# Optimization experiments

Measured on AMD Instinct MI355X. Metric: run time of the kernel, lower is better.

Reference implementation:

```python
import jax, jax.numpy as jnp
import numpy as np

K = 5  # filter_size
EPS = 1e-5

def conv1x1(x, w):
    # x: [B,Ci,H,W], w: [Co,Ci]
    return jnp.einsum('bihw,oi->bohw', x, w)

def layernorm_c(x, g, b):
    # LayerNorm over channel dim of NCHW (torch permutes to NHWC, norms last dim)
    m = x.mean(axis=1, keepdims=True)
    v = x.var(axis=1, keepdims=True)
    xn = (x - m) / jnp.sqrt(v + EPS)
    return xn * g[None, :, None, None] + b[None, :, None, None]

def conv3x3(x, w):
    return jax.lax.conv_general_dilated(x, w, (1, 1), [(1, 1), (1, 1)],
                                        dimension_numbers=('NCHW', 'OIHW', 'NCHW'))

def apply_dyn_filter(feat, filt):
    # feat: [B,C,H,W]; filt: [B,C*K*K,H,W] ordered as C x (K*K row-major), matching
    # torch .view(B,C,K*K,H,W) and F.unfold channel layout.
    B, C, H, W = feat.shape
    f = filt.reshape(B, C, K * K, H, W)
    p = K // 2
    fp = jnp.pad(feat, ((0, 0), (0, 0), (p, p), (p, p)))  # zero pad, same as F.unfold
    out = jnp.zeros_like(feat)
    for ki in range(K):
        for kj in range(K):
            out = out + fp[:, :, ki:ki + H, kj:kj + W] * f[:, :, ki * K + kj]
    return out


def setup_inputs() -> dict:
    key = jax.random.key(0)
    ks = jax.random.split(key, 9)
    B, Cin, H, W = 1, 64, 128, 128
    Ch = 128
    s = lambda fan: 1.0 / np.sqrt(fan)
    inp = {
        'rgb_high': jax.random.normal(ks[0], (B, Cin, H, W), jnp.float32),
        'event':    jax.random.normal(ks[1], (B, Cin, H, W), jnp.float32),
        'conv_w':   jax.random.normal(ks[2], (Ch, Cin), jnp.float32) * s(Cin),
        'ln_g':     jnp.ones((Ch,), jnp.float32),
        'ln_b':     jnp.zeros((Ch,), jnp.float32),
        'df1_w':    jax.random.normal(ks[3], (Ch, Ch, 3, 3), jnp.float32) * s(Ch * 9),
        'df2_w':    jax.random.normal(ks[4], (Ch * K * K, Ch), jnp.float32) * s(Ch),
        'sp_w':     jax.random.normal(ks[5], (Ch, Ch), jnp.float32) * s(Ch),
        'out_w':    jax.random.normal(ks[6], (Cin, Ch), jnp.float32) * s(Ch),
    }
    return inp


def reference(rgb_high, event, conv_w, ln_g, ln_b, df1_w, df2_w, sp_w, out_w):
    rgb_feat = layernorm_c(conv1x1(rgb_high, conv_w), ln_g, ln_b)
    ev_feat = layernorm_c(conv1x1(event, conv_w), ln_g, ln_b)
    # dynamic filter generator: conv3x3 -> ReLU -> conv1x1 (shared weights)
    rgb_filter = conv1x1(jax.nn.relu(conv3x3(rgb_feat, df1_w)), df2_w)
    ev_filter = conv1x1(jax.nn.relu(conv3x3(ev_feat, df1_w)), df2_w)
    rgb_en = apply_dyn_filter(rgb_feat, rgb_filter)
    ev_en = apply_dyn_filter(ev_feat, ev_filter)
    rgb_filtered = rgb_en * jax.nn.sigmoid(conv1x1(ev_en, sp_w))
    rgb_fused = rgb_en + rgb_filtered + rgb_feat
    rgb_norm = layernorm_c(rgb_fused, ln_g, ln_b)
    return conv1x1(rgb_norm, out_w)
```

## Files before the change

kernel.cpp:

```cpp
#include <hip/hip_runtime.h>
#include <math.h>

#define HW 16384
#define WD 128
#define HD 128
#define CIN 64
#define CH 128
#define EPSV 1e-5f

typedef __attribute__((ext_vector_type(8))) short short8;
typedef __attribute__((ext_vector_type(4))) short short4v;
typedef __attribute__((ext_vector_type(4))) float f32x4;

__device__ __forceinline__ short f2bf(float x) {
  unsigned u = __float_as_uint(x);
  u += 0x7FFFu + ((u >> 16) & 1u);
  return (short)(u >> 16);
}
__device__ __forceinline__ float bf2f(short x) {
  return __uint_as_float(((unsigned)(unsigned short)x) << 16);
}

__global__ __launch_bounds__(256) void k_prep_all(
    const float* __restrict__ cw, const float* __restrict__ w3,
    const float* __restrict__ spw, const float* __restrict__ outw,
    const float* __restrict__ rgb, const float* __restrict__ ev,
    const float* __restrict__ df2,
    short* __restrict__ cwp, short* __restrict__ w3p,
    short* __restrict__ spwp, short* __restrict__ outwp,
    short* __restrict__ xT_rgb, short* __restrict__ xT_ev,
    short* __restrict__ df2p) {
  int idx = blockIdx.x * 256 + threadIdx.x;
  if (idx < 8192) {
    int j = idx & 7, grp = (idx >> 3) & 3, m = (idx >> 5) & 127, q = idx >> 12;
    cwp[idx] = f2bf(cw[m * CIN + q * 32 + grp * 8 + j]);
  } else if (idx < 155648) {
    int i = idx - 8192;
    int j = i & 7, grp = (i >> 3) & 3, m = (i >> 5) & 127, ks = i >> 12;
    int tap = ks >> 2, q = ks & 3;
    int c = q * 32 + grp * 8 + j;
    w3p[i] = f2bf(w3[(m * CH + c) * 9 + tap]);
  } else if (idx < 172032) {
    int i = idx - 155648;
    int j = i & 7, grp = (i >> 3) & 3, m = (i >> 5) & 127, q = i >> 12;
    spwp[i] = f2bf(spw[m * CH + q * 32 + grp * 8 + j]);
  } else if (idx < 180224) {
    int i = idx - 172032;
    int j = i & 7, grp = (i >> 3) & 3, m = (i >> 5) & 63, q = i >> 11;
    outwp[i] = f2bf(outw[m * CH + q * 32 + grp * 8 + j]);
  } else if (idx < 212992) {
    int i = idx - 180224;
    int img = i >> 14, p = i & 16383;
    const float* x = img ? ev : rgb;
    short* xT = img ? xT_ev : xT_rgb;
#pragma unroll
    for (int cb = 0; cb < 8; ++cb) {
      short8 v;
#pragma unroll
      for (int j = 0; j < 8; ++j) v[j] = f2bf(x[(cb * 8 + j) * HW + p]);
      *(short8*)(xT + p * CIN + cb * 8) = v;
    }
  } else {
    int i = idx - 212992;
    int j = i & 7;
    int slotp = (i >> 3) & 511;
    int c = i >> 12;
    int t = slotp >> 4, k8l = slotp & 15;
    int k8 = k8l ^ (t & 7);
    float v = (t < 25) ? df2[(c * 25 + t) * CH + k8 * 8 + j] : 0.f;
    df2p[i] = f2bf(v);
  }
}

__global__ __launch_bounds__(256) void k_feat_mfma(
    const short* __restrict__ xT_rgb, const short* __restrict__ xT_ev,
    const short* __restrict__ cwp, const float* __restrict__ g,
    const float* __restrict__ b,
    short* __restrict__ featT_rgb, short* __restrict__ featT_ev) {
  __shared__ float sg[CH], sb[CH];
  int tid = threadIdx.x;
  if (tid < CH) { sg[tid] = g[tid]; sb[tid] = b[tid]; }
  __syncthreads();
  const short* xT = blockIdx.z ? xT_ev : xT_rgb;
  short* featT = blockIdx.z ? featT_ev : featT_rgb;
  int wave = tid >> 6, lane = tid & 63, col = lane & 15, grp = lane >> 4;
  int p = blockIdx.x * 64 + wave * 16 + col;

  const short8* bp = (const short8*)(xT + p * CIN);
  short8 bq0 = bp[grp], bq1 = bp[4 + grp];
  const short8* ap = (const short8*)cwp;

  f32x4 acc[8];
#pragma unroll
  for (int mt = 0; mt < 8; ++mt) {
    acc[mt] = (f32x4){0.f, 0.f, 0.f, 0.f};
    short8 a0 = ap[(0 * 128 + mt * 16 + col) * 4 + grp];
    short8 a1 = ap[(1 * 128 + mt * 16 + col) * 4 + grp];
    acc[mt] = __builtin_amdgcn_mfma_f32_16x16x32_bf16(a0, bq0, acc[mt], 0, 0, 0);
    acc[mt] = __builtin_amdgcn_mfma_f32_16x16x32_bf16(a1, bq1, acc[mt], 0, 0, 0);
  }
  float s = 0.f, s2 = 0.f;
#pragma unroll
  for (int mt = 0; mt < 8; ++mt)
#pragma unroll
    for (int r = 0; r < 4; ++r) { float v = acc[mt][r]; s += v; s2 += v * v; }
  s += __shfl_xor(s, 16);  s += __shfl_xor(s, 32);
  s2 += __shfl_xor(s2, 16); s2 += __shfl_xor(s2, 32);
  float mean = s * (1.f / CH);
  float var = s2 * (1.f / CH) - mean * mean;
  float rinv = rsqrtf(var + EPSV);
#pragma unroll
  for (int mt = 0; mt < 8; ++mt) {
    short4v fv;
#pragma unroll
    for (int r = 0; r < 4; ++r) {
      int m = mt * 16 + grp * 4 + r;
      fv[r] = f2bf((acc[mt][r] - mean) * rinv * sg[m] + sb[m]);
    }
    *(short4v*)(featT + p * CH + mt * 16 + grp * 4) = fv;
  }
}

__global__ __launch_bounds__(256) void k_conv3_v3(
    const short* __restrict__ featT_rgb, const short* __restrict__ featT_ev,
    const short* __restrict__ w3p,
    short* __restrict__ rT_rgb, short* __restrict__ rT_ev) {
  const short* featT = blockIdx.z ? featT_ev : featT_rgb;
  short* rT = blockIdx.z ? rT_ev : rT_rgb;
  int tid = threadIdx.x, wave = tid >> 6, lane = tid & 63;
  int col = lane & 15, grp = lane >> 4;
  int mh = wave & 1;
  int ty = (blockIdx.x >> 3) * 4 + (wave >> 1) * 2;
  int tx = (blockIdx.x & 7) * 16;
  int x = tx + col;

  f32x4 acc[2][4];
#pragma unroll
  for (int s = 0; s < 2; ++s)
#pragma unroll
    for (int mt = 0; mt < 4; ++mt) acc[s][mt] = (f32x4){0.f, 0.f, 0.f, 0.f};

  const short8* ap = (const short8*)w3p;
#pragma unroll
  for (int ks = 0; ks < 36; ++ks) {
    const int tap = ks >> 2, q = ks & 3;
    const int dy = tap / 3 - 1, dx = tap % 3 - 1;
    int xs = x + dx;
    bool xok = (unsigned)xs < (unsigned)WD;
    int y0 = ty + dy, y1 = ty + 1 + dy;
    short8 b0 = {0, 0, 0, 0, 0, 0, 0, 0}, b1 = {0, 0, 0, 0, 0, 0, 0, 0};
    if (xok && (unsigned)y0 < (unsigned)HD)
      b0 = *(const short8*)(featT + (y0 * WD + xs) * CH + q * 32 + grp * 8);
    if (xok && (unsigned)y1 < (unsigned)HD)
      b1 = *(const short8*)(featT + (y1 * WD + xs) * CH + q * 32 + grp * 8);
#pragma unroll
    for (int mt = 0; mt < 4; ++mt) {
      short8 a = ap[(ks * 128 + (mh * 4 + mt) * 16 + col) * 4 + grp];
      acc[0][mt] = __builtin_amdgcn_mfma_f32_16x16x32_bf16(a, b0, acc[0][mt], 0, 0, 0);
      acc[1][mt] = __builtin_amdgcn_mfma_f32_16x16x32_bf16(a, b1, acc[1][mt], 0, 0, 0);
    }
  }
#pragma unroll
  for (int s = 0; s < 2; ++s) {
    int p = (ty + s) * WD + x;
#pragma unroll
    for (int mt = 0; mt < 4; ++mt) {
      short4v v;
#pragma unroll
      for (int r = 0; r < 4; ++r) v[r] = f2bf(fmaxf(acc[s][mt][r], 0.f));
      *(short4v*)(rT + p * CH + (mh * 4 + mt) * 16 + grp * 4) = v;
    }
  }
}

__global__ __launch_bounds__(256, 3) void k_filt_v6(
    const short* __restrict__ featT_rgb, const short* __restrict__ featT_ev,
    const short* __restrict__ rT_rgb, const short* __restrict__ rT_ev,
    const short* __restrict__ df2p,
    short* __restrict__ enT_rgb, short* __restrict__ enT_ev) {
  __shared__ short lsA[4 * 512 * 8];
  __shared__ float fwv[4 * 400 + 64];
  const short* featT = blockIdx.z ? featT_ev : featT_rgb;
  const short* rT = blockIdx.z ? rT_ev : rT_rgb;
  short* enT = blockIdx.z ? enT_ev : enT_rgb;
  int tid = threadIdx.x;
  int wave = tid >> 6, lane = tid & 63;
  int col = lane & 15, grp = lane >> 4;
  int ty0 = (blockIdx.x >> 3) * 16, tx0 = (blockIdx.x & 7) * 16;
  int c0 = blockIdx.y * 4;
  int py0 = ty0 + wave * 4;
  int pxx = tx0 + col;

  {
    const short8* gsrc = (const short8*)(df2p + (size_t)c0 * 4096);
    short8* lA = (short8*)lsA;
    for (int i = tid; i < 2048; i += 256) lA[i] = gsrc[i];
  }
  for (int px = tid; px < 400; px += 256) {
    int wr = px / 20, wc = px % 20;
    int y = ty0 + wr - 2, x = tx0 + wc - 2;
    short4v v = {0, 0, 0, 0};
    if ((unsigned)y < (unsigned)HD && (unsigned)x < (unsigned)WD)
      v = *(const short4v*)(featT + (y * WD + x) * CH + c0);
#pragma unroll
    for (int ci = 0; ci < 4; ++ci) fwv[ci * 400 + px] = bf2f(v[ci]);
  }
  if (tid < 64) fwv[4 * 400 + tid] = 0.f;

  short8 rv[4][4];
#pragma unroll
  for (int s = 0; s < 4; ++s) {
    const short8* bp = (const short8*)(rT + ((py0 + s) * WD + pxx) * CH);
#pragma unroll
    for (int q = 0; q < 4; ++q) rv[s][q] = bp[q * 4 + grp];
  }
#pragma unroll
  for (int s = 0; s < 4; ++s)
#pragma unroll
    for (int q = 0; q < 4; ++q) asm volatile("" :: "v"(rv[s][q]));

  int idx0[4], idx1[4];
#pragma unroll
  for (int r = 0; r < 4; ++r) {
    int tap0 = grp * 4 + r;
    int tap1 = 16 + grp * 4 + r;
    idx0[r] = (wave * 4 + tap0 / 5) * 20 + col + tap0 % 5;
    idx1[r] = (wave * 4 + tap1 / 5) * 20 + col + tap1 % 5;
  }
  __syncthreads();

  const short8* lA8 = (const short8*)lsA;
  short* stp = enT + ((py0 + grp) * WD + pxx) * CH + c0;
  short4v sv;

#pragma unroll
  for (int c = 0; c < 4; ++c) {
    int base0 = c * 512 + col * 16;
    int base1 = base0 + 256;
    short8 a[4];
    f32x4 acc0[4], acc1[4];
#pragma unroll
    for (int q = 0; q < 4; ++q) a[q] = lA8[base0 + (((q << 2) | grp) ^ (col & 7))];
#pragma unroll
    for (int s = 0; s < 4; ++s) {
      acc0[s] = (f32x4){0.f, 0.f, 0.f, 0.f};
#pragma unroll
      for (int q = 0; q < 4; ++q)
        acc0[s] = __builtin_amdgcn_mfma_f32_16x16x32_bf16(a[q], rv[s][q], acc0[s], 0, 0, 0);
    }
#pragma unroll
    for (int q = 0; q < 4; ++q) a[q] = lA8[base1 + (((q << 2) | grp) ^ (col & 7))];
#pragma unroll
    for (int s = 0; s < 4; ++s) {
      acc1[s] = (f32x4){0.f, 0.f, 0.f, 0.f};
#pragma unroll
      for (int q = 0; q < 4; ++q)
        acc1[s] = __builtin_amdgcn_mfma_f32_16x16x32_bf16(a[q], rv[s][q], acc1[s], 0, 0, 0);
    }
    const float* fwc = fwv + c * 400;
    float part[4];
#pragma unroll
    for (int s = 0; s < 4; ++s) {
      float p = 0.f;
#pragma unroll
      for (int r = 0; r < 4; ++r) {
        p += fwc[idx0[r] + s * 20] * acc0[s][r];
        p += fwc[idx1[r] + s * 20] * acc1[s][r];
      }
      part[s] = p;
    }
#pragma unroll
    for (int s = 0; s < 4; ++s) part[s] += __shfl_xor(part[s], 16);
#pragma unroll
    for (int s = 0; s < 4; ++s) part[s] += __shfl_xor(part[s], 32);
    float val = (grp == 0) ? part[0] : (grp == 1) ? part[1]
              : (grp == 2) ? part[2] : part[3];
    sv[c] = f2bf(val);
  }
  *(short4v*)stp = sv;
}

__global__ __launch_bounds__(256) void k_post(
    const short* __restrict__ enT_rgb, const short* __restrict__ enT_ev,
    const short* __restrict__ featT_rgb,
    const short* __restrict__ spwp, const short* __restrict__ outwp,
    const float* __restrict__ g, const float* __restrict__ b,
    float* __restrict__ out) {
  __shared__ short nlds[4][16 * 136];
  __shared__ float sg[CH], sb[CH];
  int tid = threadIdx.x;
  if (tid < CH) { sg[tid] = g[tid]; sb[tid] = b[tid]; }
  __syncthreads();
  int wave = tid >> 6, lane = tid & 63, col = lane & 15, grp = lane >> 4;
  int p = blockIdx.x * 64 + wave * 16 + col;

  const short8* bp = (const short8*)(enT_ev + p * CH);
  short8 bq[4];
#pragma unroll
  for (int q = 0; q < 4; ++q) bq[q] = bp[q * 4 + grp];
  const short8* ap = (const short8*)spwp;
  f32x4 z[8];
#pragma unroll
  for (int mt = 0; mt < 8; ++mt) {
    z[mt] = (f32x4){0.f, 0.f, 0.f, 0.f};
#pragma unroll
    for (int q = 0; q < 4; ++q)
      z[mt] = __builtin_amdgcn_mfma_f32_16x16x32_bf16(
          ap[(q * 128 + mt * 16 + col) * 4 + grp], bq[q], z[mt], 0, 0, 0);
  }

  const short4v* er = (const short4v*)(enT_rgb + p * CH);
  const short4v* fr = (const short4v*)(featT_rgb + p * CH);
  float fused[8][4];
  float s = 0.f, s2 = 0.f;
#pragma unroll
  for (int mt = 0; mt < 8; ++mt) {
    short4v e4 = er[mt * 4 + grp];
    short4v f4 = fr[mt * 4 + grp];
#pragma unroll
    for (int r = 0; r < 4; ++r) {
      float sig = 1.f / (1.f + __expf(-z[mt][r]));
      float f = bf2f(e4[r]) * (1.f + sig) + bf2f(f4[r]);
      fused[mt][r] = f; s += f; s2 += f * f;
    }
  }
  s += __shfl_xor(s, 16);  s += __shfl_xor(s, 32);
  s2 += __shfl_xor(s2, 16); s2 += __shfl_xor(s2, 32);
  float mean = s * (1.f / CH);
  float var = s2 * (1.f / CH) - mean * mean;
  float rinv = rsqrtf(var + EPSV);

  short* nl = &nlds[wave][0];
#pragma unroll
  for (int mt = 0; mt < 8; ++mt) {
    short4v nv;
#pragma unroll
    for (int r = 0; r < 4; ++r) {
      int o = mt * 16 + grp * 4 + r;
      nv[r] = f2bf((fused[mt][r] - mean) * rinv * sg[o] + sb[o]);
    }
    *(short4v*)(nl + col * 136 + mt * 16 + grp * 4) = nv;
  }

  short8 nb[4];
#pragma unroll
  for (int q = 0; q < 4; ++q)
    nb[q] = *(const short8*)(nl + col * 136 + q * 32 + grp * 8);
  const short8* op = (const short8*)outwp;
#pragma unroll
  for (int mt = 0; mt < 4; ++mt) {
    f32x4 oacc = {0.f, 0.f, 0.f, 0.f};
#pragma unroll
    for (int q = 0; q < 4; ++q)
      oacc = __builtin_amdgcn_mfma_f32_16x16x32_bf16(
          op[(q * 64 + mt * 16 + col) * 4 + grp], nb[q], oacc, 0, 0, 0);
#pragma unroll
    for (int r = 0; r < 4; ++r)
      out[(mt * 16 + grp * 4 + r) * HW + p] = oacc[r];
  }
}

extern "C" void kernel_launch(void* const* d_in, const int* in_sizes, int n_in,
                              void* d_out, int out_size, void* d_ws, size_t ws_size,
                              hipStream_t stream) {
  const float* rgb  = (const float*)d_in[0];
  const float* ev   = (const float*)d_in[1];
  const float* cw   = (const float*)d_in[2];
  const float* g    = (const float*)d_in[3];
  const float* b    = (const float*)d_in[4];
  const float* w3   = (const float*)d_in[5];
  const float* df2  = (const float*)d_in[6];
  const float* spw  = (const float*)d_in[7];
  const float* outw = (const float*)d_in[8];
  float* out = (float*)d_out;
  char* wsb = (char*)d_ws;

  const size_t MB = 1u << 20;
  short* featT_rgb = (short*)(wsb);
  short* featT_ev  = (short*)(wsb + 4 * MB);
  short* rT_rgb    = (short*)(wsb + 8 * MB);
  short* rT_ev     = (short*)(wsb + 12 * MB);
  short* enT_rgb   = (short*)(wsb + 16 * MB);
  short* enT_ev    = (short*)(wsb + 20 * MB);
  short* xT_rgb    = (short*)(wsb + 24 * MB);
  short* xT_ev     = (short*)(wsb + 26 * MB);
  short* df2p      = (short*)(wsb + 28 * MB);
  short* w3p       = (short*)(wsb + 29 * MB);
  short* cwp       = (short*)(wsb + 30 * MB);
  short* spwp      = (short*)(wsb + 31 * MB);
  short* outwp     = (short*)(wsb + 32 * MB);

  hipLaunchKernelGGL(k_prep_all, dim3(2880), dim3(256), 0, stream,
                     cw, w3, spw, outw, rgb, ev, df2,
                     cwp, w3p, spwp, outwp, xT_rgb, xT_ev, df2p);
  hipLaunchKernelGGL(k_feat_mfma, dim3(256, 1, 2), dim3(256), 0, stream,
                     xT_rgb, xT_ev, cwp, g, b, featT_rgb, featT_ev);
  hipLaunchKernelGGL(k_conv3_v3, dim3(256, 1, 2), dim3(256), 0, stream,
                     featT_rgb, featT_ev, w3p, rT_rgb, rT_ev);
  hipLaunchKernelGGL(k_filt_v6, dim3(64, 32, 2), dim3(256), 0, stream,
                     featT_rgb, featT_ev, rT_rgb, rT_ev, df2p, enT_rgb, enT_ev);
  hipLaunchKernelGGL(k_post, dim3(256), dim3(256), 0, stream,
                     enT_rgb, enT_ev, featT_rgb, spwp, outwp, g, b, out);
}
```

Before: 113.4 us.

## Switch dynamic-filter kernel to 32x32x16 MFMA with repacked tap layout

Rewrites the filter-generation-and-apply kernel to use 32x32x16 bf16 MFMA instead of 16x16x32. The 25 filter taps are repacked into 32 rows in a new order chosen to match the 32x32 output layout, and the B-operand loads cover two pixel rows per tile. The per-lane tap-weighted reduction now needs only one cross-lane shuffle instead of two, with fewer accumulator registers per output. The intent is higher MFMA throughput and less reduction and shuffle overhead. In exchange the tap indexing becomes harder to follow and more register tiles live at once.

```diff
diff --git a/kernel.cpp b/kernel.cpp
--- a/kernel.cpp
+++ b/kernel.cpp
@@ -11,6 +11,7 @@
 typedef __attribute__((ext_vector_type(8))) short short8;
 typedef __attribute__((ext_vector_type(4))) short short4v;
 typedef __attribute__((ext_vector_type(4))) float f32x4;
+typedef __attribute__((ext_vector_type(16))) float f32x16;
 
 __device__ __forceinline__ short f2bf(float x) {
   unsigned u = __float_as_uint(x);
@@ -65,9 +66,15 @@
     int j = i & 7;
     int slotp = (i >> 3) & 511;
     int c = i >> 12;
-    int t = slotp >> 4, k8l = slotp & 15;
-    int k8 = k8l ^ (t & 7);
-    float v = (t < 25) ? df2[(c * 25 + t) * CH + k8 * 8 + j] : 0.f;
+    int m = slotp >> 4, k8s = slotp & 15;
+    int k8 = k8s ^ (m & 7);
+    int k = k8 * 8 + j;
+    int t;
+    if (m < 20) t = (m >> 2) * 5 + (m & 3);
+    else if (m == 24) t = 24;
+    else if (m >= 28) t = (m - 28) * 5 + 4;
+    else t = -1;
+    float v = (t >= 0) ? df2[(c * 25 + t) * CH + k] : 0.f;
     df2p[i] = f2bf(v);
   }
 }
@@ -173,23 +180,25 @@
   }
 }
 
-__global__ __launch_bounds__(256, 3) void k_filt_v6(
+__global__ __launch_bounds__(256, 3) void k_filt_v11(
     const short* __restrict__ featT_rgb, const short* __restrict__ featT_ev,
     const short* __restrict__ rT_rgb, const short* __restrict__ rT_ev,
     const short* __restrict__ df2p,
     short* __restrict__ enT_rgb, short* __restrict__ enT_ev) {
   __shared__ short lsA[4 * 512 * 8];
-  __shared__ float fwv[4 * 400 + 64];
+  __shared__ float fwv[4 * 400];
   const short* featT = blockIdx.z ? featT_ev : featT_rgb;
   const short* rT = blockIdx.z ? rT_ev : rT_rgb;
   short* enT = blockIdx.z ? enT_ev : enT_rgb;
   int tid = threadIdx.x;
   int wave = tid >> 6, lane = tid & 63;
-  int col = lane & 15, grp = lane >> 4;
+  int hi = lane >> 5;
+  int n = lane & 31;
+  int rbit = (n >> 4) & 1;
+  int cc = n & 15;
   int ty0 = (blockIdx.x >> 3) * 16, tx0 = (blockIdx.x & 7) * 16;
   int c0 = blockIdx.y * 4;
   int py0 = ty0 + wave * 4;
-  int pxx = tx0 + col;
 
   {
     const short8* gsrc = (const short8*)(df2p + (size_t)c0 * 4096);
@@ -205,77 +214,62 @@
 #pragma unroll
     for (int ci = 0; ci < 4; ++ci) fwv[ci * 400 + px] = bf2f(v[ci]);
   }
-  if (tid < 64) fwv[4 * 400 + tid] = 0.f;
-
-  short8 rv[4][4];
-#pragma unroll
-  for (int s = 0; s < 4; ++s) {
-    const short8* bp = (const short8*)(rT + ((py0 + s) * WD + pxx) * CH);
-#pragma unroll
-    for (int q = 0; q < 4; ++q) rv[s][q] = bp[q * 4 + grp];
-  }
-#pragma unroll
-  for (int s = 0; s < 4; ++s)
-#pragma unroll
-    for (int q = 0; q < 4; ++q) asm volatile("" :: "v"(rv[s][q]));
-
-  int idx0[4], idx1[4];
-#pragma unroll
-  for (int r = 0; r < 4; ++r) {
-    int tap0 = grp * 4 + r;
-    int tap1 = 16 + grp * 4 + r;
-    idx0[r] = (wave * 4 + tap0 / 5) * 20 + col + tap0 % 5;
-    idx1[r] = (wave * 4 + tap1 / 5) * 20 + col + tap1 % 5;
-  }
+
+  short8 rv[2][8];
+#pragma unroll
+  for (int P = 0; P < 2; ++P) {
+    const short* bsrc = rT + ((py0 + 2 * P + rbit) * WD + tx0 + cc) * CH + hi * 8;
+#pragma unroll
+    for (int ks = 0; ks < 8; ++ks)
+      rv[P][ks] = *(const short8*)(bsrc + ks * 16);
+  }
+#pragma unroll
+  for (int P = 0; P < 2; ++P)
+#pragma unroll
+    for (int ks = 0; ks < 8; ++ks) asm volatile("" :: "v"(rv[P][ks]));
+
+  int fwb0 = (wave * 4 + rbit) * 20 + cc;
+  int q0o = 20 * hi;
+  int q1o = 40 + 20 * hi;
+  int q2o = hi ? 0 : 80;
+  int s0o = hi ? 4 : 84;
+  int s1o = hi ? 24 : 84;
+  int s2o = hi ? 44 : 84;
+  int s3o = hi ? 64 : 84;
   __syncthreads();
 
   const short8* lA8 = (const short8*)lsA;
-  short* stp = enT + ((py0 + grp) * WD + pxx) * CH + c0;
+  int sw = n & 7;
+  short* stp = enT + ((py0 + 2 * hi + rbit) * WD + tx0 + cc) * CH + c0;
   short4v sv;
 
 #pragma unroll
   for (int c = 0; c < 4; ++c) {
-    int base0 = c * 512 + col * 16;
-    int base1 = base0 + 256;
-    short8 a[4];
-    f32x4 acc0[4], acc1[4];
-#pragma unroll
-    for (int q = 0; q < 4; ++q) a[q] = lA8[base0 + (((q << 2) | grp) ^ (col & 7))];
-#pragma unroll
-    for (int s = 0; s < 4; ++s) {
-      acc0[s] = (f32x4){0.f, 0.f, 0.f, 0.f};
-#pragma unroll
-      for (int q = 0; q < 4; ++q)
-        acc0[s] = __builtin_amdgcn_mfma_f32_16x16x32_bf16(a[q], rv[s][q], acc0[s], 0, 0, 0);
-    }
-#pragma unroll
-    for (int q = 0; q < 4; ++q) a[q] = lA8[base1 + (((q << 2) | grp) ^ (col & 7))];
-#pragma unroll
-    for (int s = 0; s < 4; ++s) {
-      acc1[s] = (f32x4){0.f, 0.f, 0.f, 0.f};
-#pragma unroll
-      for (int q = 0; q < 4; ++q)
-        acc1[s] = __builtin_amdgcn_mfma_f32_16x16x32_bf16(a[q], rv[s][q], acc1[s], 0, 0, 0);
-    }
-    const float* fwc = fwv + c * 400;
-    float part[4];
-#pragma unroll
-    for (int s = 0; s < 4; ++s) {
-      float p = 0.f;
-#pragma unroll
-      for (int r = 0; r < 4; ++r) {
-        p += fwc[idx0[r] + s * 20] * acc0[s][r];
-        p += fwc[idx1[r] + s * 20] * acc1[s][r];
-      }
-      part[s] = p;
-    }
-#pragma unroll
-    for (int s = 0; s < 4; ++s) part[s] += __shfl_xor(part[s], 16);
-#pragma unroll
-    for (int s = 0; s < 4; ++s) part[s] += __shfl_xor(part[s], 32);
-    float val = (grp == 0) ? part[0] : (grp == 1) ? part[1]
-              : (grp == 2) ? part[2] : part[3];
-    sv[c] = f2bf(val);
+    short8 a[8];
+#pragma unroll
+    for (int ks = 0; ks < 8; ++ks)
+      a[ks] = lA8[c * 512 + n * 16 + ((ks * 2 + hi) ^ sw)];
+    float vals[2];
+#pragma unroll
+    for (int P = 0; P < 2; ++P) {
+      f32x16 acc = {0.f, 0.f, 0.f, 0.f, 0.f, 0.f, 0.f, 0.f,
+                    0.f, 0.f, 0.f, 0.f, 0.f, 0.f, 0.f, 0.f};
+#pragma unroll
+      for (int ks = 0; ks < 8; ++ks)
+        acc = __builtin_amdgcn_mfma_f32_32x32x16_bf16(a[ks], rv[P][ks], acc, 0, 0, 0);
+      const float* fwc = fwv + c * 400 + fwb0 + P * 40;
+      float v = fwc[q0o]     * acc[0]  + fwc[q0o + 1] * acc[1]
+              + fwc[q0o + 2] * acc[2]  + fwc[q0o + 3] * acc[3]
+              + fwc[q1o]     * acc[4]  + fwc[q1o + 1] * acc[5]
+              + fwc[q1o + 2] * acc[6]  + fwc[q1o + 3] * acc[7]
+              + fwc[q2o]     * acc[8]  + fwc[q2o + 1] * acc[9]
+              + fwc[q2o + 2] * acc[10] + fwc[q2o + 3] * acc[11]
+              + fwc[s0o] * acc[12] + fwc[s1o] * acc[13]
+              + fwc[s2o] * acc[14] + fwc[s3o] * acc[15];
+      v += __shfl_xor(v, 32);
+      vals[P] = v;
+    }
+    sv[c] = f2bf(hi ? vals[1] : vals[0]);
   }
   *(short4v*)stp = sv;
 }
@@ -397,7 +391,7 @@
                      xT_rgb, xT_ev, cwp, g, b, featT_rgb, featT_ev);
   hipLaunchKernelGGL(k_conv3_v3, dim3(256, 1, 2), dim3(256), 0, stream,
                      featT_rgb, featT_ev, w3p, rT_rgb, rT_ev);
-  hipLaunchKernelGGL(k_filt_v6, dim3(64, 32, 2), dim3(256), 0, stream,
+  hipLaunchKernelGGL(k_filt_v11, dim3(64, 32, 2), dim3(256), 0, stream,
                      featT_rgb, featT_ev, rT_rgb, rT_ev, df2p, enT_rgb, enT_ev);
   hipLaunchKernelGGL(k_post, dim3(256), dim3(256), 0, stream,
                      enT_rgb, enT_ev, featT_rgb, spwp, outwp, g, b, out);
```

New measurement: 135.5 us. 19.5% more time.
